# Kernel optimization log

Measured on AMD Instinct MI355X. Metric: run time of the kernel, lower is better.

The kernel has to match this reference:

```python
import jax, jax.numpy as jnp
import numpy as np

DEPTH, HEADS, DFF = 64, 8, 256
T_FINAL, DT = 1.0, 0.25
NEG_INF = -1e9


def setup_inputs() -> dict:
    key = jax.random.key(0)
    ks = jax.random.split(key, 8)
    B, S, d = 4, 512, DEPTH

    def p(k, shp):
        return jax.random.normal(k, shp, jnp.float32) * (1.0 / np.sqrt(shp[0]).astype(np.float32))

    return {
        "x": jax.random.normal(ks[0], (B, S, d), jnp.float32),
        "mask": jnp.zeros((B, 1, S, 1), jnp.float32),  # additive float mask, 0 = keep
        "Wq": p(ks[1], (d, d)), "bq": jnp.zeros((d,), jnp.float32),
        "Wk": p(ks[2], (d, d)), "bk": jnp.zeros((d,), jnp.float32),
        "Wv": p(ks[3], (d, d)), "bv": jnp.zeros((d,), jnp.float32),
        "Wo": p(ks[4], (d, d)), "bo": jnp.zeros((d,), jnp.float32),
        "W1": p(ks[5], (d, DFF)), "b1": jnp.zeros((DFF,), jnp.float32),
        "W2": p(ks[6], (DFF, d)), "b2": jnp.zeros((d,), jnp.float32),
    }


def _mha(y, mask, Wq, bq, Wk, bk, Wv, bv, Wo, bo):
    B, S, d = y.shape
    H, dh = HEADS, d // HEADS

    def split(z):  # [B,S,d] -> [B,H,S,dh]
        return z.reshape(B, S, H, dh).transpose(0, 2, 1, 3)

    q = split(y @ Wq + bq)
    k = split(y @ Wk + bk)
    v = split(y @ Wv + bv)
    scores = jnp.einsum('bhqd,bhkd->bhqk', q, k) / jnp.sqrt(jnp.asarray(dh, jnp.float32))
    scores = scores + mask * NEG_INF  # mask [B,1,S,1] broadcasts over key axis
    attn = jax.nn.softmax(scores, axis=-1)
    out = jnp.einsum('bhqk,bhkd->bhqd', attn, v)
    out = out.transpose(0, 2, 1, 3).reshape(B, S, d)
    return out @ Wo + bo


def reference(x, mask, Wq, bq, Wk, bk, Wv, bv, Wo, bo, W1, b1, W2, b2):
    def ffn(h):
        return jnp.maximum(h @ W1 + b1, 0.0) @ W2 + b2

    def dyn(y):  # ALBERT dynamics: dx/dt = Attn(x) + FFN(x + Attn(x))
        att = _mha(y, mask, Wq, bq, Wk, bk, Wv, bv, Wo, bo)
        return att + ffn(y + att)

    @jax.checkpoint
    def step(y, _):  # one RKF56 (Fehlberg 6-stage, 5th-order) fixed step
        k1 = dyn(y)
        k2 = dyn(y + DT * (0.25 * k1))
        k3 = dyn(y + DT * (3.0/32.0 * k1 + 9.0/32.0 * k2))
        k4 = dyn(y + DT * (1932.0/2197.0 * k1 - 7200.0/2197.0 * k2 + 7296.0/2197.0 * k3))
        k5 = dyn(y + DT * (439.0/216.0 * k1 - 8.0 * k2 + 3680.0/513.0 * k3 - 845.0/4104.0 * k4))
        k6 = dyn(y + DT * (-8.0/27.0 * k1 + 2.0 * k2 - 3544.0/2565.0 * k3 + 1859.0/4104.0 * k4 - 11.0/40.0 * k5))
        y_next = y + DT * (16.0/135.0 * k1 + 6656.0/12825.0 * k3 + 28561.0/56430.0 * k4 - 9.0/50.0 * k5 + 2.0/55.0 * k6)
        return y_next, None

    n_steps = int(round(T_FINAL / DT))
    y, _ = jax.lax.scan(step, x, None, length=n_steps)
    return y
```

## Files before the change

### kernel.cpp

```cpp
#include <hip/hip_runtime.h>

#define B_    4
#define S_    512
#define D_    64
#define DFF_  256
#define N_    2048
#define GWG   256
#define TPB   512
#define RPW   8
#define NSTEPS 4
#define DTs   0.25f

__constant__ float A_tab[6][5] = {
    {0.f, 0.f, 0.f, 0.f, 0.f},
    {0.25f, 0.f, 0.f, 0.f, 0.f},
    {3.0f/32.0f, 9.0f/32.0f, 0.f, 0.f, 0.f},
    {1932.0f/2197.0f, -7200.0f/2197.0f, 7296.0f/2197.0f, 0.f, 0.f},
    {439.0f/216.0f, -8.0f, 3680.0f/513.0f, -845.0f/4104.0f, 0.f},
    {-8.0f/27.0f, 2.0f, -3544.0f/2565.0f, 1859.0f/4104.0f, -11.0f/40.0f}};
__constant__ float B_tab[6] = {16.0f/135.0f, 0.0f, 6656.0f/12825.0f,
                               28561.0f/56430.0f, -9.0f/50.0f, 2.0f/55.0f};

__global__ __launch_bounds__(TPB, 1) void proj0_kernel(
    const float* __restrict__ x,
    const float* __restrict__ Wq, const float* __restrict__ bq,
    const float* __restrict__ Wk, const float* __restrict__ bk,
    const float* __restrict__ Wv, const float* __restrict__ bv,
    float* __restrict__ g_y, float* __restrict__ g_sy, float* __restrict__ g_q,
    float* __restrict__ g_k, float* __restrict__ g_v)
{
    const int wg   = blockIdx.x;
    const int tid  = threadIdx.x;
    const int lane = tid & 63;
    const int wv   = tid >> 6;
    const int sid  = (wg & 7) * 32 + (wg >> 3);
    const int row0 = sid * RPW;
    const int r_own = wv, c_own = lane;
    const size_t idx = (size_t)(row0 + r_own) * D_ + c_own;

    __shared__ float sy[RPW][D_];
    __shared__ float U[3072];

    const float yv = x[idx];
    g_y[idx]  = yv;
    g_sy[idx] = yv;
    sy[r_own][c_own] = yv;
    __syncthreads();

    if (wv < 6) {
        const int mat = wv >> 1, p = wv & 1;
        const float* Wm = (mat == 0) ? Wq : (mat == 1) ? Wk : Wv;
        float acc[8];
        #pragma unroll
        for (int r = 0; r < 8; ++r) acc[r] = 0.f;
        #pragma unroll
        for (int i4 = 0; i4 < 8; ++i4) {
            const int dd0 = p * 32 + i4 * 4;
            const float w0 = Wm[(dd0 + 0) * D_ + lane];
            const float w1 = Wm[(dd0 + 1) * D_ + lane];
            const float w2 = Wm[(dd0 + 2) * D_ + lane];
            const float w3 = Wm[(dd0 + 3) * D_ + lane];
            #pragma unroll
            for (int r = 0; r < 8; ++r) {
                const float4 s4 = *(const float4*)&sy[r][dd0];
                acc[r] = fmaf(s4.x, w0, fmaf(s4.y, w1, fmaf(s4.z, w2, fmaf(s4.w, w3, acc[r]))));
            }
        }
        #pragma unroll
        for (int r = 0; r < 8; ++r) U[(wv * 8 + r) * 64 + lane] = acc[r];
    }
    __syncthreads();

    {
        const float qv = U[(0 * 8 + r_own) * 64 + c_own] + U[(1 * 8 + r_own) * 64 + c_own] + bq[c_own];
        const float kv = U[(2 * 8 + r_own) * 64 + c_own] + U[(3 * 8 + r_own) * 64 + c_own] + bk[c_own];
        const float vv = U[(4 * 8 + r_own) * 64 + c_own] + U[(5 * 8 + r_own) * 64 + c_own] + bv[c_own];
        g_q[idx] = qv * 0.51006702f;
        g_k[idx] = kv;
        g_v[idx] = vv;
    }
}

__global__ __launch_bounds__(TPB, 1) void fused_kernel(
    const float* __restrict__ Wq, const float* __restrict__ bq,
    const float* __restrict__ Wk, const float* __restrict__ bk,
    const float* __restrict__ Wv, const float* __restrict__ bv,
    const float* __restrict__ Wo, const float* __restrict__ bo,
    const float* __restrict__ W1, const float* __restrict__ b1,
    const float* __restrict__ W2, const float* __restrict__ b2,
    float* __restrict__ out,
    float* __restrict__ g_y,  float* __restrict__ g_sy, float* __restrict__ g_q,
    float* __restrict__ g_k,  float* __restrict__ g_v,  float* __restrict__ g_kst,
    const int t)
{
    const int wg   = blockIdx.x;
    const int tid  = threadIdx.x;
    const int lane = tid & 63;
    const int wv   = tid >> 6;
    const int sid  = (wg & 7) * 32 + (wg >> 3);
    const int row0  = sid * RPW;
    const int krow0 = (sid >> 6) * S_;
    const int stage = t % 6;
    const int step  = t / 6;
    const int buf   = t & 1;

    const int r_own = wv, c_own = lane;
    const size_t idx = (size_t)(row0 + r_own) * D_ + c_own;

    __shared__ float satt[RPW][D_];
    __shared__ float sh[RPW][D_];
    __shared__ float st[RPW][DFF_];
    __shared__ float sy[RPW][D_];
    __shared__ float U[5120];

    {
        const int h = lane & 7;
        const int r = lane >> 3;
        float qv[8];
        {
            const float* qrow = g_q + (size_t)(row0 + r) * D_ + h * 8;
            const float4 qa = *(const float4*)qrow;
            const float4 qb = *(const float4*)(qrow + 4);
            qv[0] = qa.x; qv[1] = qa.y; qv[2] = qa.z; qv[3] = qa.w;
            qv[4] = qb.x; qv[5] = qb.y; qv[6] = qb.z; qv[7] = qb.w;
        }
        const float* kb = g_k + ((size_t)buf * N_ + krow0 + wv * 64) * D_ + h * 8;
        const float* vb = g_v + ((size_t)buf * N_ + krow0 + wv * 64) * D_ + h * 8;

        float m = -1e30f, l = 0.f;
        float acc8[8];
        #pragma unroll
        for (int d = 0; d < 8; ++d) acc8[d] = 0.f;

        for (int j0 = 0; j0 < 64; j0 += 4) {
            float4 kA[4], kB[4], vA[4], vB[4];
            #pragma unroll
            for (int u = 0; u < 4; ++u) {
                const float* kr = kb + (size_t)(j0 + u) * D_;
                kA[u] = *(const float4*)kr;
                kB[u] = *(const float4*)(kr + 4);
            }
            #pragma unroll
            for (int u = 0; u < 4; ++u) {
                const float* vr = vb + (size_t)(j0 + u) * D_;
                vA[u] = *(const float4*)vr;
                vB[u] = *(const float4*)(vr + 4);
            }
            float s0, s1, s2, s3;
            s0 = fmaf(qv[0],kA[0].x,fmaf(qv[1],kA[0].y,fmaf(qv[2],kA[0].z,fmaf(qv[3],kA[0].w,
                 fmaf(qv[4],kB[0].x,fmaf(qv[5],kB[0].y,fmaf(qv[6],kB[0].z,qv[7]*kB[0].w)))))));
            s1 = fmaf(qv[0],kA[1].x,fmaf(qv[1],kA[1].y,fmaf(qv[2],kA[1].z,fmaf(qv[3],kA[1].w,
                 fmaf(qv[4],kB[1].x,fmaf(qv[5],kB[1].y,fmaf(qv[6],kB[1].z,qv[7]*kB[1].w)))))));
            s2 = fmaf(qv[0],kA[2].x,fmaf(qv[1],kA[2].y,fmaf(qv[2],kA[2].z,fmaf(qv[3],kA[2].w,
                 fmaf(qv[4],kB[2].x,fmaf(qv[5],kB[2].y,fmaf(qv[6],kB[2].z,qv[7]*kB[2].w)))))));
            s3 = fmaf(qv[0],kA[3].x,fmaf(qv[1],kA[3].y,fmaf(qv[2],kA[3].z,fmaf(qv[3],kA[3].w,
                 fmaf(qv[4],kB[3].x,fmaf(qv[5],kB[3].y,fmaf(qv[6],kB[3].z,qv[7]*kB[3].w)))))));

            const float bm = fmaxf(fmaxf(s0, s1), fmaxf(s2, s3));
            if (bm > m + 8.f) {
                const float al = exp2f(m - bm);
                m = bm; l *= al;
                #pragma unroll
                for (int d = 0; d < 8; ++d) acc8[d] *= al;
            }
            const float p0 = exp2f(s0 - m);
            const float p1 = exp2f(s1 - m);
            const float p2 = exp2f(s2 - m);
            const float p3 = exp2f(s3 - m);
            l += (p0 + p1) + (p2 + p3);
            acc8[0] = fmaf(p0,vA[0].x,fmaf(p1,vA[1].x,fmaf(p2,vA[2].x,fmaf(p3,vA[3].x,acc8[0]))));
            acc8[1] = fmaf(p0,vA[0].y,fmaf(p1,vA[1].y,fmaf(p2,vA[2].y,fmaf(p3,vA[3].y,acc8[1]))));
            acc8[2] = fmaf(p0,vA[0].z,fmaf(p1,vA[1].z,fmaf(p2,vA[2].z,fmaf(p3,vA[3].z,acc8[2]))));
            acc8[3] = fmaf(p0,vA[0].w,fmaf(p1,vA[1].w,fmaf(p2,vA[2].w,fmaf(p3,vA[3].w,acc8[3]))));
            acc8[4] = fmaf(p0,vB[0].x,fmaf(p1,vB[1].x,fmaf(p2,vB[2].x,fmaf(p3,vB[3].x,acc8[4]))));
            acc8[5] = fmaf(p0,vB[0].y,fmaf(p1,vB[1].y,fmaf(p2,vB[2].y,fmaf(p3,vB[3].y,acc8[5]))));
            acc8[6] = fmaf(p0,vB[0].z,fmaf(p1,vB[1].z,fmaf(p2,vB[2].z,fmaf(p3,vB[3].z,acc8[6]))));
            acc8[7] = fmaf(p0,vB[0].w,fmaf(p1,vB[1].w,fmaf(p2,vB[2].w,fmaf(p3,vB[3].w,acc8[7]))));
        }
        const int pb = ((wv * 8 + r) * 8 + h) * 10;
        #pragma unroll
        for (int d = 0; d < 8; ++d) U[pb + d] = acc8[d];
        U[pb + 8] = m;
        U[pb + 9] = l;
    }
    __syncthreads();

    {
        const int h = c_own >> 3, d = c_own & 7;
        float M = -1e30f, L = 0.f, A = 0.f;
        #pragma unroll
        for (int w = 0; w < 8; ++w) {
            const int pb = ((w * 8 + r_own) * 8 + h) * 10;
            const float mm = U[pb + 8];
            const float ll = U[pb + 9];
            const float aa = U[pb + d];
            const float Mn = fmaxf(M, mm);
            const float f  = exp2f(M - Mn);
            const float g  = exp2f(mm - Mn);
            L = L * f + ll * g;
            A = A * f + aa * g;
            M = Mn;
        }
        satt[r_own][c_own] = A * __builtin_amdgcn_rcpf(L);
    }
    __syncthreads();

    {
        float acc[8];
        #pragma unroll
        for (int r = 0; r < 8; ++r) acc[r] = 0.f;
        #pragma unroll
        for (int i4 = 0; i4 < 2; ++i4) {
            const int dd0 = wv * 8 + i4 * 4;
            const float w0 = Wo[(dd0 + 0) * D_ + lane];
            const float w1 = Wo[(dd0 + 1) * D_ + lane];
            const float w2 = Wo[(dd0 + 2) * D_ + lane];
            const float w3 = Wo[(dd0 + 3) * D_ + lane];
            #pragma unroll
            for (int r = 0; r < 8; ++r) {
                const float4 s4 = *(const float4*)&satt[r][dd0];
                acc[r] = fmaf(s4.x, w0, fmaf(s4.y, w1, fmaf(s4.z, w2, fmaf(s4.w, w3, acc[r]))));
            }
        }
        #pragma unroll
        for (int r = 0; r < 8; ++r) U[(wv * 8 + r) * 64 + lane] = acc[r];
    }
    __syncthreads();

    float so_reg, stin;
    {
        stin = g_sy[idx];
        float a = 0.f;
        #pragma unroll
        for (int w = 0; w < 8; ++w) a += U[(w * 8 + r_own) * 64 + c_own];
        so_reg = a + bo[c_own];
        sh[r_own][c_own] = stin + so_reg;
    }
    __syncthreads();

    {
        const int c2 = tid & 255, p = tid >> 8;
        float acc[8];
        #pragma unroll
        for (int r = 0; r < 8; ++r) acc[r] = 0.f;
        #pragma unroll
        for (int i4 = 0; i4 < 8; ++i4) {
            const int dd0 = p * 32 + i4 * 4;
            const float w0 = W1[(dd0 + 0) * DFF_ + c2];
            const float w1 = W1[(dd0 + 1) * DFF_ + c2];
            const float w2 = W1[(dd0 + 2) * DFF_ + c2];
            const float w3 = W1[(dd0 + 3) * DFF_ + c2];
            #pragma unroll
            for (int r = 0; r < 8; ++r) {
                const float4 s4 = *(const float4*)&sh[r][dd0];
                acc[r] = fmaf(s4.x, w0, fmaf(s4.y, w1, fmaf(s4.z, w2, fmaf(s4.w, w3, acc[r]))));
            }
        }
        #pragma unroll
        for (int r = 0; r < 8; ++r) U[(p * 8 + r) * 256 + c2] = acc[r];
    }
    __syncthreads();

    {
        const int c2 = tid & 255, rbase = (tid >> 8) * 4;
        const float b1c = b1[c2];
        #pragma unroll
        for (int i = 0; i < 4; ++i) {
            const int r = rbase + i;
            st[r][c2] = fmaxf(U[r * 256 + c2] + U[(8 + r) * 256 + c2] + b1c, 0.f);
        }
    }
    __syncthreads();

    {
        float acc[8];
        #pragma unroll
        for (int r = 0; r < 8; ++r) acc[r] = 0.f;
        #pragma unroll
        for (int i4 = 0; i4 < 8; ++i4) {
            const int cc0 = wv * 32 + i4 * 4;
            const float w0 = W2[(cc0 + 0) * D_ + lane];
            const float w1 = W2[(cc0 + 1) * D_ + lane];
            const float w2 = W2[(cc0 + 2) * D_ + lane];
            const float w3 = W2[(cc0 + 3) * D_ + lane];
            #pragma unroll
            for (int r = 0; r < 8; ++r) {
                const float4 s4 = *(const float4*)&st[r][cc0];
                acc[r] = fmaf(s4.x, w0, fmaf(s4.y, w1, fmaf(s4.z, w2, fmaf(s4.w, w3, acc[r]))));
            }
        }
        #pragma unroll
        for (int r = 0; r < 8; ++r) U[(wv * 8 + r) * 64 + lane] = acc[r];
    }
    __syncthreads();

    float sn = 0.f;
    {
        float f = 0.f;
        #pragma unroll
        for (int w = 0; w < 8; ++w) f += U[(w * 8 + r_own) * 64 + c_own];
        const float kv = so_reg + f + b2[c_own];

        float kj0 = 0.f, kj1 = 0.f, kj2 = 0.f, kj3 = 0.f, kj4 = 0.f;
        if (0 < stage) kj0 = g_kst[0 * (size_t)N_ * D_ + idx];
        if (1 < stage) kj1 = g_kst[1 * (size_t)N_ * D_ + idx];
        if (2 < stage) kj2 = g_kst[2 * (size_t)N_ * D_ + idx];
        if (3 < stage) kj3 = g_kst[3 * (size_t)N_ * D_ + idx];
        if (4 < stage) kj4 = g_kst[4 * (size_t)N_ * D_ + idx];
        kj0 = (stage == 0) ? kv : kj0;
        kj1 = (stage == 1) ? kv : kj1;
        kj2 = (stage == 2) ? kv : kj2;
        kj3 = (stage == 3) ? kv : kj3;
        kj4 = (stage == 4) ? kv : kj4;

        float yv = g_y[idx];
        if (stage < 5) {
            g_kst[(size_t)stage * N_ * D_ + idx] = kv;
        } else {
            float yn = B_tab[0] * kj0;
            yn = fmaf(B_tab[2], kj2, yn);
            yn = fmaf(B_tab[3], kj3, yn);
            yn = fmaf(B_tab[4], kj4, yn);
            yn = fmaf(B_tab[5], kv, yn);
            yn = fmaf(DTs, yn, yv);
            if (step == NSTEPS - 1) { out[idx] = yn; return; }
            g_y[idx] = yn;
            yv = yn;
        }
        const int ns = (stage < 5) ? stage + 1 : 0;
        sn = yv;
        sn = fmaf(DTs * A_tab[ns][0], kj0, sn);
        sn = fmaf(DTs * A_tab[ns][1], kj1, sn);
        sn = fmaf(DTs * A_tab[ns][2], kj2, sn);
        sn = fmaf(DTs * A_tab[ns][3], kj3, sn);
        sn = fmaf(DTs * A_tab[ns][4], kj4, sn);
        g_sy[idx] = sn;
        sy[r_own][c_own] = sn;
    }
    __syncthreads();

    if (wv < 6) {
        const int mat = wv >> 1, p = wv & 1;
        const float* Wm = (mat == 0) ? Wq : (mat == 1) ? Wk : Wv;
        float acc[8];
        #pragma unroll
        for (int r = 0; r < 8; ++r) acc[r] = 0.f;
        #pragma unroll
        for (int i4 = 0; i4 < 8; ++i4) {
            const int dd0 = p * 32 + i4 * 4;
            const float w0 = Wm[(dd0 + 0) * D_ + lane];
            const float w1 = Wm[(dd0 + 1) * D_ + lane];
            const float w2 = Wm[(dd0 + 2) * D_ + lane];
            const float w3 = Wm[(dd0 + 3) * D_ + lane];
            #pragma unroll
            for (int r = 0; r < 8; ++r) {
                const float4 s4 = *(const float4*)&sy[r][dd0];
                acc[r] = fmaf(s4.x, w0, fmaf(s4.y, w1, fmaf(s4.z, w2, fmaf(s4.w, w3, acc[r]))));
            }
        }
        #pragma unroll
        for (int r = 0; r < 8; ++r) U[(wv * 8 + r) * 64 + lane] = acc[r];
    }
    __syncthreads();

    {
        const float qv = U[(0 * 8 + r_own) * 64 + c_own] + U[(1 * 8 + r_own) * 64 + c_own] + bq[c_own];
        const float kv = U[(2 * 8 + r_own) * 64 + c_own] + U[(3 * 8 + r_own) * 64 + c_own] + bk[c_own];
        const float vv = U[(4 * 8 + r_own) * 64 + c_own] + U[(5 * 8 + r_own) * 64 + c_own] + bv[c_own];
        g_q[idx] = qv * 0.51006702f;
        const size_t kidx = ((size_t)(buf ^ 1) * N_ + row0 + r_own) * D_ + c_own;
        g_k[kidx] = kv;
        g_v[kidx] = vv;
    }
}

extern "C" void kernel_launch(void* const* d_in, const int* in_sizes, int n_in,
                              void* d_out, int out_size, void* d_ws, size_t ws_size,
                              hipStream_t stream) {
    const float* x  = (const float*)d_in[0];
    const float* Wq = (const float*)d_in[2];
    const float* bq = (const float*)d_in[3];
    const float* Wk = (const float*)d_in[4];
    const float* bk = (const float*)d_in[5];
    const float* Wv = (const float*)d_in[6];
    const float* bv = (const float*)d_in[7];
    const float* Wo = (const float*)d_in[8];
    const float* bo = (const float*)d_in[9];
    const float* W1 = (const float*)d_in[10];
    const float* b1 = (const float*)d_in[11];
    const float* W2 = (const float*)d_in[12];
    const float* b2 = (const float*)d_in[13];
    float* out  = (float*)d_out;

    float* base = (float*)d_ws;
    float* g_y   = base;
    float* g_sy  = g_y  + (size_t)N_ * D_;
    float* g_q   = g_sy + (size_t)N_ * D_;
    float* g_k   = g_q  + (size_t)N_ * D_;
    float* g_v   = g_k  + 2 * (size_t)N_ * D_;
    float* g_kst = g_v  + 2 * (size_t)N_ * D_;

    hipLaunchKernelGGL(proj0_kernel, dim3(GWG), dim3(TPB), 0, stream,
                       x, Wq, bq, Wk, bk, Wv, bv, g_y, g_sy, g_q, g_k, g_v);
    for (int t = 0; t < 24; ++t) {
        hipLaunchKernelGGL(fused_kernel, dim3(GWG), dim3(TPB), 0, stream,
                           Wq, bq, Wk, bk, Wv, bv, Wo, bo, W1, b1, W2, b2,
                           out, g_y, g_sy, g_q, g_k, g_v, g_kst, t);
    }
}
```

Baseline: 552.6 us.

## Halve rows per workgroup and double grid, splitting attention keys across wave halves

```diff
diff --git a/kernel.cpp b/kernel.cpp
--- a/kernel.cpp
+++ b/kernel.cpp
@@ -5,9 +5,9 @@
 #define D_    64
 #define DFF_  256
 #define N_    2048
-#define GWG   256
+#define GWG   512
 #define TPB   512
-#define RPW   8
+#define RPW   4
 #define NSTEPS 4
 #define DTs   0.25f
 
@@ -33,26 +33,29 @@
     const int tid  = threadIdx.x;
     const int lane = tid & 63;
     const int wv   = tid >> 6;
-    const int sid  = (wg & 7) * 32 + (wg >> 3);
+    const int sid  = (wg & 7) * 64 + (wg >> 3);
     const int row0 = sid * RPW;
-    const int r_own = wv, c_own = lane;
+    const int r_own = tid >> 6;
+    const int c_own = lane;
     const size_t idx = (size_t)(row0 + r_own) * D_ + c_own;
 
     __shared__ float sy[RPW][D_];
-    __shared__ float U[3072];
-
-    const float yv = x[idx];
-    g_y[idx]  = yv;
-    g_sy[idx] = yv;
-    sy[r_own][c_own] = yv;
+    __shared__ float U[1536];
+
+    if (tid < 256) {
+        const float yv = x[idx];
+        g_y[idx]  = yv;
+        g_sy[idx] = yv;
+        sy[r_own][c_own] = yv;
+    }
     __syncthreads();
 
     if (wv < 6) {
         const int mat = wv >> 1, p = wv & 1;
         const float* Wm = (mat == 0) ? Wq : (mat == 1) ? Wk : Wv;
-        float acc[8];
-        #pragma unroll
-        for (int r = 0; r < 8; ++r) acc[r] = 0.f;
+        float acc[RPW];
+        #pragma unroll
+        for (int r = 0; r < RPW; ++r) acc[r] = 0.f;
         #pragma unroll
         for (int i4 = 0; i4 < 8; ++i4) {
             const int dd0 = p * 32 + i4 * 4;
@@ -61,20 +64,20 @@
             const float w2 = Wm[(dd0 + 2) * D_ + lane];
             const float w3 = Wm[(dd0 + 3) * D_ + lane];
             #pragma unroll
-            for (int r = 0; r < 8; ++r) {
+            for (int r = 0; r < RPW; ++r) {
                 const float4 s4 = *(const float4*)&sy[r][dd0];
                 acc[r] = fmaf(s4.x, w0, fmaf(s4.y, w1, fmaf(s4.z, w2, fmaf(s4.w, w3, acc[r]))));
             }
         }
         #pragma unroll
-        for (int r = 0; r < 8; ++r) U[(wv * 8 + r) * 64 + lane] = acc[r];
-    }
-    __syncthreads();
-
-    {
-        const float qv = U[(0 * 8 + r_own) * 64 + c_own] + U[(1 * 8 + r_own) * 64 + c_own] + bq[c_own];
-        const float kv = U[(2 * 8 + r_own) * 64 + c_own] + U[(3 * 8 + r_own) * 64 + c_own] + bk[c_own];
-        const float vv = U[(4 * 8 + r_own) * 64 + c_own] + U[(5 * 8 + r_own) * 64 + c_own] + bv[c_own];
+        for (int r = 0; r < RPW; ++r) U[(wv * RPW + r) * 64 + lane] = acc[r];
+    }
+    __syncthreads();
+
+    if (tid < 256) {
+        const float qv = U[(0 * RPW + r_own) * 64 + c_own] + U[(1 * RPW + r_own) * 64 + c_own] + bq[c_own];
+        const float kv = U[(2 * RPW + r_own) * 64 + c_own] + U[(3 * RPW + r_own) * 64 + c_own] + bk[c_own];
+        const float vv = U[(4 * RPW + r_own) * 64 + c_own] + U[(5 * RPW + r_own) * 64 + c_own] + bv[c_own];
         g_q[idx] = qv * 0.51006702f;
         g_k[idx] = kv;
         g_v[idx] = vv;
@@ -97,14 +100,15 @@
     const int tid  = threadIdx.x;
     const int lane = tid & 63;
     const int wv   = tid >> 6;
-    const int sid  = (wg & 7) * 32 + (wg >> 3);
+    const int sid  = (wg & 7) * 64 + (wg >> 3);
     const int row0  = sid * RPW;
-    const int krow0 = (sid >> 6) * S_;
+    const int krow0 = (sid >> 7) * S_;
     const int stage = t % 6;
     const int step  = t / 6;
     const int buf   = t & 1;
 
-    const int r_own = wv, c_own = lane;
+    const int r_own = tid >> 6;
+    const int c_own = lane;
     const size_t idx = (size_t)(row0 + r_own) * D_ + c_own;
 
     __shared__ float satt[RPW][D_];
@@ -114,8 +118,10 @@
     __shared__ float U[5120];
 
     {
-        const int h = lane & 7;
-        const int r = lane >> 3;
+        const int h    = lane & 7;
+        const int rh   = lane >> 3;
+        const int r    = rh & 3;
+        const int half = rh >> 2;
         float qv[8];
         {
             const float* qrow = g_q + (size_t)(row0 + r) * D_ + h * 8;
@@ -124,15 +130,15 @@
             qv[0] = qa.x; qv[1] = qa.y; qv[2] = qa.z; qv[3] = qa.w;
             qv[4] = qb.x; qv[5] = qb.y; qv[6] = qb.z; qv[7] = qb.w;
         }
-        const float* kb = g_k + ((size_t)buf * N_ + krow0 + wv * 64) * D_ + h * 8;
-        const float* vb = g_v + ((size_t)buf * N_ + krow0 + wv * 64) * D_ + h * 8;
+        const float* kb = g_k + ((size_t)buf * N_ + krow0 + wv * 64 + half * 32) * D_ + h * 8;
+        const float* vb = g_v + ((size_t)buf * N_ + krow0 + wv * 64 + half * 32) * D_ + h * 8;
 
         float m = -1e30f, l = 0.f;
         float acc8[8];
         #pragma unroll
         for (int d = 0; d < 8; ++d) acc8[d] = 0.f;
 
-        for (int j0 = 0; j0 < 64; j0 += 4) {
+        for (int j0 = 0; j0 < 32; j0 += 4) {
             float4 kA[4], kB[4], vA[4], vB[4];
             #pragma unroll
             for (int u = 0; u < 4; ++u) {
@@ -177,7 +183,7 @@
             acc8[6] = fmaf(p0,vB[0].z,fmaf(p1,vB[1].z,fmaf(p2,vB[2].z,fmaf(p3,vB[3].z,acc8[6]))));
             acc8[7] = fmaf(p0,vB[0].w,fmaf(p1,vB[1].w,fmaf(p2,vB[2].w,fmaf(p3,vB[3].w,acc8[7]))));
         }
-        const int pb = ((wv * 8 + r) * 8 + h) * 10;
+        const int pb = (((wv * 2 + half) * 4 + r) * 8 + h) * 10;
         #pragma unroll
         for (int d = 0; d < 8; ++d) U[pb + d] = acc8[d];
         U[pb + 8] = m;
@@ -185,12 +191,12 @@
     }
     __syncthreads();
 
-    {
+    if (tid < 256) {
         const int h = c_own >> 3, d = c_own & 7;
         float M = -1e30f, L = 0.f, A = 0.f;
         #pragma unroll
-        for (int w = 0; w < 8; ++w) {
-            const int pb = ((w * 8 + r_own) * 8 + h) * 10;
+        for (int w = 0; w < 16; ++w) {
+            const int pb = ((w * 4 + r_own) * 8 + h) * 10;
             const float mm = U[pb + 8];
             const float ll = U[pb + 9];
             const float aa = U[pb + d];
@@ -206,9 +212,9 @@
     __syncthreads();
 
     {
-        float acc[8];
-        #pragma unroll
-        for (int r = 0; r < 8; ++r) acc[r] = 0.f;
+        float acc[RPW];
+        #pragma unroll
+        for (int r = 0; r < RPW; ++r) acc[r] = 0.f;
         #pragma unroll
         for (int i4 = 0; i4 < 2; ++i4) {
             const int dd0 = wv * 8 + i4 * 4;
@@ -217,22 +223,22 @@
             const float w2 = Wo[(dd0 + 2) * D_ + lane];
             const float w3 = Wo[(dd0 + 3) * D_ + lane];
             #pragma unroll
-            for (int r = 0; r < 8; ++r) {
+            for (int r = 0; r < RPW; ++r) {
                 const float4 s4 = *(const float4*)&satt[r][dd0];
                 acc[r] = fmaf(s4.x, w0, fmaf(s4.y, w1, fmaf(s4.z, w2, fmaf(s4.w, w3, acc[r]))));
             }
         }
         #pragma unroll
-        for (int r = 0; r < 8; ++r) U[(wv * 8 + r) * 64 + lane] = acc[r];
-    }
-    __syncthreads();
-
-    float so_reg, stin;
-    {
+        for (int r = 0; r < RPW; ++r) U[(wv * RPW + r) * 64 + lane] = acc[r];
+    }
+    __syncthreads();
+
+    float so_reg = 0.f, stin = 0.f;
+    if (tid < 256) {
         stin = g_sy[idx];
         float a = 0.f;
         #pragma unroll
-        for (int w = 0; w < 8; ++w) a += U[(w * 8 + r_own) * 64 + c_own];
+        for (int w = 0; w < 8; ++w) a += U[(w * RPW + r_own) * 64 + c_own];
         so_reg = a + bo[c_own];
         sh[r_own][c_own] = stin + so_reg;
     }
@@ -240,9 +246,9 @@
 
     {
         const int c2 = tid & 255, p = tid >> 8;
-        float acc[8];
-        #pragma unroll
-        for (int r = 0; r < 8; ++r) acc[r] = 0.f;
+        float acc[RPW];
+        #pragma unroll
+        for (int r = 0; r < RPW; ++r) acc[r] = 0.f;
         #pragma unroll
         for (int i4 = 0; i4 < 8; ++i4) {
             const int dd0 = p * 32 + i4 * 4;
@@ -251,31 +257,31 @@
             const float w2 = W1[(dd0 + 2) * DFF_ + c2];
             const float w3 = W1[(dd0 + 3) * DFF_ + c2];
             #pragma unroll
-            for (int r = 0; r < 8; ++r) {
+            for (int r = 0; r < RPW; ++r) {
                 const float4 s4 = *(const float4*)&sh[r][dd0];
                 acc[r] = fmaf(s4.x, w0, fmaf(s4.y, w1, fmaf(s4.z, w2, fmaf(s4.w, w3, acc[r]))));
             }
         }
         #pragma unroll
-        for (int r = 0; r < 8; ++r) U[(p * 8 + r) * 256 + c2] = acc[r];
+        for (int r = 0; r < RPW; ++r) U[(p * RPW + r) * 256 + c2] = acc[r];
     }
     __syncthreads();
 
     {
-        const int c2 = tid & 255, rbase = (tid >> 8) * 4;
+        const int c2 = tid & 255, rb = (tid >> 8) * 2;
         const float b1c = b1[c2];
         #pragma unroll
-        for (int i = 0; i < 4; ++i) {
-            const int r = rbase + i;
-            st[r][c2] = fmaxf(U[r * 256 + c2] + U[(8 + r) * 256 + c2] + b1c, 0.f);
+        for (int i = 0; i < 2; ++i) {
+            const int r = rb + i;
+            st[r][c2] = fmaxf(U[r * 256 + c2] + U[(RPW + r) * 256 + c2] + b1c, 0.f);
         }
     }
     __syncthreads();
 
     {
-        float acc[8];
-        #pragma unroll
-        for (int r = 0; r < 8; ++r) acc[r] = 0.f;
+        float acc[RPW];
+        #pragma unroll
+        for (int r = 0; r < RPW; ++r) acc[r] = 0.f;
         #pragma unroll
         for (int i4 = 0; i4 < 8; ++i4) {
             const int cc0 = wv * 32 + i4 * 4;
@@ -284,24 +290,24 @@
             const float w2 = W2[(cc0 + 2) * D_ + lane];
             const float w3 = W2[(cc0 + 3) * D_ + lane];
             #pragma unroll
-            for (int r = 0; r < 8; ++r) {
+            for (int r = 0; r < RPW; ++r) {
                 const float4 s4 = *(const float4*)&st[r][cc0];
                 acc[r] = fmaf(s4.x, w0, fmaf(s4.y, w1, fmaf(s4.z, w2, fmaf(s4.w, w3, acc[r]))));
             }
         }
         #pragma unroll
-        for (int r = 0; r < 8; ++r) U[(wv * 8 + r) * 64 + lane] = acc[r];
-    }
-    __syncthreads();
-
-    float sn = 0.f;
-    {
+        for (int r = 0; r < RPW; ++r) U[(wv * RPW + r) * 64 + lane] = acc[r];
+    }
+    __syncthreads();
+
+    float sn = 0.f, yn = 0.f;
+    float kj0 = 0.f, kj1 = 0.f, kj2 = 0.f, kj3 = 0.f, kj4 = 0.f, yv = 0.f;
+    if (tid < 256) {
         float f = 0.f;
         #pragma unroll
-        for (int w = 0; w < 8; ++w) f += U[(w * 8 + r_own) * 64 + c_own];
+        for (int w = 0; w < 8; ++w) f += U[(w * RPW + r_own) * 64 + c_own];
         const float kv = so_reg + f + b2[c_own];
 
-        float kj0 = 0.f, kj1 = 0.f, kj2 = 0.f, kj3 = 0.f, kj4 = 0.f;
         if (0 < stage) kj0 = g_kst[0 * (size_t)N_ * D_ + idx];
         if (1 < stage) kj1 = g_kst[1 * (size_t)N_ * D_ + idx];
         if (2 < stage) kj2 = g_kst[2 * (size_t)N_ * D_ + idx];
@@ -313,20 +319,24 @@
         kj3 = (stage == 3) ? kv : kj3;
         kj4 = (stage == 4) ? kv : kj4;
 
-        float yv = g_y[idx];
+        yv = g_y[idx];
         if (stage < 5) {
             g_kst[(size_t)stage * N_ * D_ + idx] = kv;
         } else {
-            float yn = B_tab[0] * kj0;
+            yn = B_tab[0] * kj0;
             yn = fmaf(B_tab[2], kj2, yn);
             yn = fmaf(B_tab[3], kj3, yn);
             yn = fmaf(B_tab[4], kj4, yn);
             yn = fmaf(B_tab[5], kv, yn);
             yn = fmaf(DTs, yn, yv);
-            if (step == NSTEPS - 1) { out[idx] = yn; return; }
-            g_y[idx] = yn;
+            if (step == NSTEPS - 1) out[idx] = yn;
+            else                    g_y[idx] = yn;
             yv = yn;
         }
+    }
+    if (t == NSTEPS * 6 - 1) return;
+
+    if (tid < 256) {
         const int ns = (stage < 5) ? stage + 1 : 0;
         sn = yv;
         sn = fmaf(DTs * A_tab[ns][0], kj0, sn);
@@ -342,9 +352,9 @@
     if (wv < 6) {
         const int mat = wv >> 1, p = wv & 1;
         const float* Wm = (mat == 0) ? Wq : (mat == 1) ? Wk : Wv;
-        float acc[8];
-        #pragma unroll
-        for (int r = 0; r < 8; ++r) acc[r] = 0.f;
+        float acc[RPW];
+        #pragma unroll
+        for (int r = 0; r < RPW; ++r) acc[r] = 0.f;
         #pragma unroll
         for (int i4 = 0; i4 < 8; ++i4) {
             const int dd0 = p * 32 + i4 * 4;
@@ -353,20 +363,20 @@
             const float w2 = Wm[(dd0 + 2) * D_ + lane];
             const float w3 = Wm[(dd0 + 3) * D_ + lane];
             #pragma unroll
-            for (int r = 0; r < 8; ++r) {
+            for (int r = 0; r < RPW; ++r) {
                 const float4 s4 = *(const float4*)&sy[r][dd0];
                 acc[r] = fmaf(s4.x, w0, fmaf(s4.y, w1, fmaf(s4.z, w2, fmaf(s4.w, w3, acc[r]))));
             }
         }
         #pragma unroll
-        for (int r = 0; r < 8; ++r) U[(wv * 8 + r) * 64 + lane] = acc[r];
-    }
-    __syncthreads();
-
-    {
-        const float qv = U[(0 * 8 + r_own) * 64 + c_own] + U[(1 * 8 + r_own) * 64 + c_own] + bq[c_own];
-        const float kv = U[(2 * 8 + r_own) * 64 + c_own] + U[(3 * 8 + r_own) * 64 + c_own] + bk[c_own];
-        const float vv = U[(4 * 8 + r_own) * 64 + c_own] + U[(5 * 8 + r_own) * 64 + c_own] + bv[c_own];
+        for (int r = 0; r < RPW; ++r) U[(wv * RPW + r) * 64 + lane] = acc[r];
+    }
+    __syncthreads();
+
+    if (tid < 256) {
+        const float qv = U[(0 * RPW + r_own) * 64 + c_own] + U[(1 * RPW + r_own) * 64 + c_own] + bq[c_own];
+        const float kv = U[(2 * RPW + r_own) * 64 + c_own] + U[(3 * RPW + r_own) * 64 + c_own] + bk[c_own];
+        const float vv = U[(4 * RPW + r_own) * 64 + c_own] + U[(5 * RPW + r_own) * 64 + c_own] + bv[c_own];
         g_q[idx] = qv * 0.51006702f;
         const size_t kidx = ((size_t)(buf ^ 1) * N_ + row0 + r_own) * D_ + c_own;
         g_k[kidx] = kv;
```

Result: no change. 554.8 us (+0.4%).
